# Kernel optimization log

Measured on AMD Instinct MI355X. Metric: run time of the kernel, lower is better.

Reference implementation:

```python
import jax, jax.numpy as jnp
import numpy as np

N = 100000       # nodes
E = 3200000      # edges
IN_DIM = 128
EDGE_DIM = 16
H = 64           # hidden_dim
L = 3            # num_layers
G = 256          # num graphs
BN_EPS = 1e-5


def setup_inputs() -> dict:
    key = jax.random.key(0)
    ks = jax.random.split(key, 16)
    x = jax.random.normal(ks[0], (N, IN_DIM), dtype=jnp.float32)
    edge_attr = jax.random.normal(ks[1], (E, EDGE_DIM), dtype=jnp.float32)
    edge_index = jax.random.randint(ks[2], (2, E), 0, N, dtype=jnp.int64)
    batch = jnp.sort(jax.random.randint(ks[3], (N,), 0, G, dtype=jnp.int64))
    s = 0.05
    np_w = jax.random.normal(ks[4], (IN_DIM, H), dtype=jnp.float32) * s
    np_b = jnp.zeros((H,), dtype=jnp.float32)
    ep_w = jax.random.normal(ks[5], (EDGE_DIM, H), dtype=jnp.float32) * s
    ep_b = jnp.zeros((H,), dtype=jnp.float32)
    mlp_w1 = jax.random.normal(ks[6], (L, H, H), dtype=jnp.float32) * s
    mlp_b1 = jnp.zeros((L, H), dtype=jnp.float32)
    mlp_w2 = jax.random.normal(ks[7], (L, H, H), dtype=jnp.float32) * s
    mlp_b2 = jnp.zeros((L, H), dtype=jnp.float32)
    bn_g = jnp.ones((L, H), dtype=jnp.float32)
    bn_b = jnp.zeros((L, H), dtype=jnp.float32)
    return {"x": x, "edge_attr": edge_attr, "edge_index": edge_index, "batch": batch,
            "np_w": np_w, "np_b": np_b, "ep_w": ep_w, "ep_b": ep_b,
            "mlp_w1": mlp_w1, "mlp_b1": mlp_b1, "mlp_w2": mlp_w2, "mlp_b2": mlp_b2,
            "bn_g": bn_g, "bn_b": bn_b}


def reference(x, edge_attr, edge_index, batch, np_w, np_b, ep_w, ep_b,
              mlp_w1, mlp_b1, mlp_w2, mlp_b2, bn_g, bn_b):
    h = x @ np_w + np_b                  # [N,H] node_proj
    e = edge_attr @ ep_w + ep_b          # [E,H] edge_proj
    src, dst = edge_index[0], edge_index[1]
    for l in range(L):
        # GINEConv (eps=0): MLP(x_i + sum_j ReLU(x_j + e_ij))
        msg = jax.nn.relu(h[src] + e)                          # [E,H] gather + edge add
        agg = jax.ops.segment_sum(msg, dst, num_segments=N)    # scatter-add
        z = h + agg
        z = jax.nn.relu(z @ mlp_w1[l] + mlp_b1[l]) @ mlp_w2[l] + mlp_b2[l]
        # BatchNorm1d over node dim (batch statistics, training-mode math)
        mu = jnp.mean(z, axis=0)
        var = jnp.mean((z - mu) ** 2, axis=0)
        z = (z - mu) * jax.lax.rsqrt(var + BN_EPS) * bn_g[l] + bn_b[l]
        h = jax.nn.relu(z)               # dropout omitted (deterministic reference)
    # global_mean_pool
    sums = jax.ops.segment_sum(h, batch, num_segments=G)
    cnts = jax.ops.segment_sum(jnp.ones((N,), dtype=h.dtype), batch, num_segments=G)
    graph_emb = sums / jnp.maximum(cnts, 1.0)[:, None]
    return h, graph_emb
```

## Files before the change

kernel.cpp:

```cpp
#include <hip/hip_runtime.h>
#include <hip/hip_bf16.h>

#define NN 100000
#define NE 3200000
#define IND 128
#define ED 16
#define HD 64
#define NL 3
#define NG 256
#define BN_EPS 1e-5f

#define NB 391
#define PBLK 512
#define PCHUNK 6250
#define MLP_BLOCKS 512

typedef unsigned int uint32;
typedef unsigned long long uint64;
typedef unsigned short ushort16;
typedef __attribute__((ext_vector_type(8))) short bf16x8;
typedef __attribute__((ext_vector_type(4))) float f32x4;

__device__ __forceinline__ ushort16 f2b(float f) {
    uint32 u = __float_as_uint(f);
    u = (u + 0x7fffu + ((u >> 16) & 1u)) >> 16;
    return (ushort16)u;
}
__device__ __forceinline__ float b2f(ushort16 b) {
    return __uint_as_float(((uint32)b) << 16);
}

__global__ __launch_bounds__(256) void k_node_proj(
    const float* __restrict__ x, const float* __restrict__ w,
    const float* __restrict__ b, ushort16* __restrict__ sb)
{
    __shared__ float xs[4][IND];
    const int wave = threadIdx.x >> 6, lane = threadIdx.x & 63;
    const int node = blockIdx.x * 4 + wave;
    const float2 v = *(const float2*)(x + (size_t)node * IND + lane * 2);
    ((float2*)xs[wave])[lane] = v;
    float acc = b[lane];
#pragma unroll
    for (int k = 0; k < IND; ++k)
        acc = fmaf(xs[wave][k], w[k * HD + lane], acc);
    sb[node * HD + lane] = f2b(acc);
}

__global__ __launch_bounds__(256) void k_p1(const int* __restrict__ ei,
                                            int* __restrict__ bh)
{
    __shared__ int hist[NB];
    const int t = threadIdx.x, blk = blockIdx.x;
    for (int i = t; i < NB; i += 256) hist[i] = 0;
    __syncthreads();
    const int base = blk * PCHUNK;
    for (int i = t; i < PCHUNK; i += 256)
        atomicAdd(&hist[ei[NE + base + i] >> 8], 1);
    __syncthreads();
    for (int i = t; i < NB; i += 256) bh[blk * NB + i] = hist[i];
}

__global__ __launch_bounds__(512) void k_p2(int* __restrict__ bh,
                                            int* __restrict__ bstart,
                                            int* __restrict__ rowptr)
{
    __shared__ int tot[NB];
    __shared__ int bsl[NB + 1];
    const int t = threadIdx.x;
    if (t < NB) {
        int s = 0;
        for (int blk = 0; blk < PBLK; ++blk) {
            const int idx = blk * NB + t;
            const int v = bh[idx];
            bh[idx] = s;
            s += v;
        }
        tot[t] = s;
    }
    __syncthreads();
    if (t == 0) {
        int run = 0;
        for (int b = 0; b < NB; ++b) { bsl[b] = run; run += tot[b]; }
        bsl[NB] = run;
    }
    __syncthreads();
    if (t < NB) {
        const int base = bsl[t];
        for (int blk = 0; blk < PBLK; ++blk) bh[blk * NB + t] += base;
        bstart[t] = base;
    }
    if (t == 0) { bstart[NB] = NE; rowptr[NN] = NE; }
}

__global__ __launch_bounds__(256) void k_p3(const int* __restrict__ ei,
                                            const int* __restrict__ bh,
                                            uint64* __restrict__ tmp)
{
    __shared__ int cursor[NB];
    const int t = threadIdx.x, blk = blockIdx.x;
    for (int i = t; i < NB; i += 256) cursor[i] = bh[blk * NB + i];
    __syncthreads();
    const int base = blk * PCHUNK;
    for (int i = t; i < PCHUNK; i += 256) {
        const int e = base + i;
        const int d = ei[NE + e];
        const int s = ei[e];
        const int pos = atomicAdd(&cursor[d >> 8], 1);
        tmp[pos] = (uint64)(uint32)d | ((uint64)(uint32)s << 17)
                 | ((uint64)(uint32)e << 34);
    }
}

__global__ __launch_bounds__(256) void k_p4(const uint64* __restrict__ tmp,
                                            const int* __restrict__ bstart,
                                            int* __restrict__ perm_src,
                                            int* __restrict__ perm_eid,
                                            int* __restrict__ rowptr)
{
    __shared__ int cnt[256], csave[256], cnt2[256];
    const int t = threadIdx.x, b = blockIdx.x;
    const int lo = bstart[b], hi = bstart[b + 1];
    cnt[t] = 0; cnt2[t] = 0;
    __syncthreads();
    for (int e = lo + t; e < hi; e += 256)
        atomicAdd(&cnt[(int)(tmp[e] & 0x1FFFF) & 255], 1);
    __syncthreads();
    csave[t] = cnt[t];
    __syncthreads();
    for (int off = 1; off < 256; off <<= 1) {
        const int v = (t >= off) ? cnt[t - off] : 0;
        __syncthreads();
        cnt[t] += v;
        __syncthreads();
    }
    const int excl = cnt[t] - csave[t];
    const int node = (b << 8) + t;
    if (node < NN) rowptr[node] = lo + excl;
    __syncthreads();
    csave[t] = excl;
    __syncthreads();
    for (int e = lo + t; e < hi; e += 256) {
        const uint64 u = tmp[e];
        const int loc = (int)(u & 0x1FFFF) & 255;
        const int r = atomicAdd(&cnt2[loc], 1);
        const int pos = lo + csave[loc] + r;
        perm_src[pos] = (int)((u >> 17) & 0x1FFFF);
        perm_eid[pos] = (int)(u >> 34);
    }
}

__global__ __launch_bounds__(256) void k_permute(
    const float* __restrict__ ea, const int* __restrict__ perm_eid,
    ushort16* __restrict__ ea_perm)
{
    const int pos = blockIdx.x * 256 + threadIdx.x;
    const int p = pos >> 2, q = pos & 3;
    const int eid = perm_eid[p];
    const float4 v = ((const float4*)(ea + (size_t)eid * ED))[q];
    ushort4 o;
    o.x = f2b(v.x); o.y = f2b(v.y); o.z = f2b(v.z); o.w = f2b(v.w);
    ((ushort4*)ea_perm)[pos] = o;
}

template <bool XFORM>
__global__ __launch_bounds__(256) void k_gather(
    const ushort16* __restrict__ eab, const int* __restrict__ perm_src,
    const int* __restrict__ rowptr,
    const float* __restrict__ epw, const float* __restrict__ epb,
    const ushort16* __restrict__ sb, const float* __restrict__ bnp,
    float* __restrict__ z)
{
    __shared__ float pe[4][64 * 17];
    const int lane = threadIdx.x & 63;
    const int wave = threadIdx.x >> 6;
    const int l15 = lane & 15, lg = lane >> 4;

    bf16x8 bfrag[4];
#pragma unroll
    for (int c = 0; c < 4; ++c) {
#pragma unroll
        for (int i = 0; i < 8; ++i) {
            const int k = lg * 8 + i;
            short v = 0;
            if (k < ED)       v = (short)f2b(epw[k * HD + c * 16 + l15]);
            else if (k == ED) v = (short)f2b(epb[c * 16 + l15]);
            bfrag[c][i] = v;
        }
    }
    const float tsc = XFORM ? bnp[lane] : 1.f;
    const float tsh = XFORM ? bnp[64 + lane] : 0.f;
    float* mype = pe[wave];

    const int node = __builtin_amdgcn_readfirstlane((blockIdx.x << 2) + wave);
    const int rs = rowptr[node];
    const int re = rowptr[node + 1];

    float acc = 0.f;
    for (int j = rs; j < re; j += 16) {
        int s[16];
#pragma unroll
        for (int m = 0; m < 16; ++m) {
            int idx = j + m;
            if (idx > NE - 1) idx = NE - 1;
            s[m] = perm_src[idx];
        }
        float hv[16];
#pragma unroll
        for (int m = 0; m < 16; ++m)
            hv[m] = b2f(sb[(size_t)s[m] * HD + lane]);

        bf16x8 a = {};
        if (lg < 2) {
            int row = j + l15;
            if (row > NE - 1) row = NE - 1;
            a = *(const bf16x8*)((const short*)eab + (size_t)row * ED + lg * 8);
        } else if (lg == 2) {
            a[0] = (short)0x3F80;
        }

        const f32x4 zero = {0.f, 0.f, 0.f, 0.f};
#pragma unroll
        for (int c = 0; c < 4; ++c) {
            const f32x4 d = __builtin_amdgcn_mfma_f32_16x16x32_bf16(
                a, bfrag[c], zero, 0, 0, 0);
            const int base = (c * 16 + l15) * 17 + lg * 4;
#pragma unroll
            for (int v = 0; v < 4; ++v) mype[base + v] = d[v];
        }

        if (XFORM) {
#pragma unroll
            for (int m = 0; m < 16; ++m)
                hv[m] = fmaxf(fmaf(hv[m], tsc, tsh), 0.f);
        }
        const int lim = re - j;
#pragma unroll
        for (int m = 0; m < 16; ++m) {
            if (m < lim)
                acc += fmaxf(hv[m] + mype[lane * 17 + m], 0.f);
        }
    }
    float u0 = b2f(sb[(size_t)node * HD + lane]);
    if (XFORM) u0 = fmaxf(fmaf(u0, tsc, tsh), 0.f);
    z[node * HD + lane] = acc + u0;
}

template <bool STORE_BF16>
__global__ __launch_bounds__(256) void k_mlp(
    float* __restrict__ z,
    const float* __restrict__ w1, const float* __restrict__ b1,
    const float* __restrict__ w2, const float* __restrict__ b2,
    ushort16* __restrict__ sb, float* __restrict__ part)
{
    __shared__ float z0s[4][HD];
    __shared__ float t1s[4][HD];
    __shared__ float red[4][2][HD];
    const int wave = threadIdx.x >> 6, lane = threadIdx.x & 63;
    const float vb1 = b1[lane], vb2 = b2[lane];
    float s1 = 0.f, s2 = 0.f;
    for (int node = blockIdx.x * 4 + wave; node < NN; node += MLP_BLOCKS * 4) {
        const int idx = node * HD + lane;
        z0s[wave][lane] = z[idx];
        float a = vb1;
#pragma unroll
        for (int k = 0; k < HD; ++k)
            a = fmaf(z0s[wave][k], w1[k * HD + lane], a);
        a = fmaxf(a, 0.f);
        t1s[wave][lane] = a;
        float o = vb2;
#pragma unroll
        for (int k = 0; k < HD; ++k)
            o = fmaf(t1s[wave][k], w2[k * HD + lane], o);
        if (STORE_BF16) sb[idx] = f2b(o);
        else            z[idx] = o;
        s1 += o;
        s2 += o * o;
    }
    red[wave][0][lane] = s1;
    red[wave][1][lane] = s2;
    __syncthreads();
    if (wave == 0) {
        float a = red[0][0][lane] + red[1][0][lane] + red[2][0][lane] + red[3][0][lane];
        float c = red[0][1][lane] + red[1][1][lane] + red[2][1][lane] + red[3][1][lane];
        part[blockIdx.x * 128 + lane] = a;
        part[blockIdx.x * 128 + 64 + lane] = c;
    }
}

__global__ __launch_bounds__(1024) void k_bn_final(
    const float* __restrict__ part,
    const float* __restrict__ g, const float* __restrict__ b,
    float* __restrict__ bnp)
{
    __shared__ float red[16][2][HD];
    const int c = threadIdx.x & 63;
    const int s = threadIdx.x >> 6;
    float s1 = 0.f, s2 = 0.f;
    for (int i = s; i < MLP_BLOCKS; i += 16) {
        s1 += part[i * 128 + c];
        s2 += part[i * 128 + 64 + c];
    }
    red[s][0][c] = s1;
    red[s][1][c] = s2;
    __syncthreads();
    if (s == 0) {
        float a = 0.f, q = 0.f;
#pragma unroll
        for (int i = 0; i < 16; ++i) { a += red[i][0][c]; q += red[i][1][c]; }
        const float mu  = a / (float)NN;
        const float var = q / (float)NN - mu * mu;
        const float rstd = rsqrtf(var + BN_EPS);
        const float sc = rstd * g[c];
        bnp[c] = sc;
        bnp[64 + c] = b[c] - mu * sc;
    }
}

__global__ __launch_bounds__(256) void k_pool_apply(
    const float* __restrict__ t2, const float* __restrict__ bnp,
    const int* __restrict__ batch,
    float* __restrict__ h, float* __restrict__ emb)
{
    __shared__ float red[4][HD];
    const int g = blockIdx.x;
    const int lane = threadIdx.x & 63;
    const int wave = threadIdx.x >> 6;
    int lo = 0, hi = NN;
    while (lo < hi) { int m = (lo + hi) >> 1; if (batch[m] < g) lo = m + 1; else hi = m; }
    const int start = lo;
    hi = NN;
    while (lo < hi) { int m = (lo + hi) >> 1; if (batch[m] <= g) lo = m + 1; else hi = m; }
    const int end = lo;
    const float sc = bnp[lane];
    const float sh = bnp[64 + lane];
    float acc = 0.f;
    for (int n = start + wave; n < end; n += 4) {
        const float v = fmaxf(fmaf(t2[(size_t)n * HD + lane], sc, sh), 0.f);
        h[(size_t)n * HD + lane] = v;
        acc += v;
    }
    red[wave][lane] = acc;
    __syncthreads();
    if (wave == 0) {
        const float a = red[0][lane] + red[1][lane] + red[2][lane] + red[3][lane];
        emb[g * HD + lane] = a / fmaxf((float)(end - start), 1.f);
    }
}

extern "C" void kernel_launch(void* const* d_in, const int* in_sizes, int n_in,
                              void* d_out, int out_size, void* d_ws, size_t ws_size,
                              hipStream_t stream)
{
    const float* x     = (const float*)d_in[0];
    const float* ea    = (const float*)d_in[1];
    const int*   ei    = (const int*)d_in[2];
    const int*   batch = (const int*)d_in[3];
    const float* np_w  = (const float*)d_in[4];
    const float* np_b  = (const float*)d_in[5];
    const float* ep_w  = (const float*)d_in[6];
    const float* ep_b  = (const float*)d_in[7];
    const float* w1    = (const float*)d_in[8];
    const float* b1    = (const float*)d_in[9];
    const float* w2    = (const float*)d_in[10];
    const float* b2    = (const float*)d_in[11];
    const float* bng   = (const float*)d_in[12];
    const float* bnb   = (const float*)d_in[13];

    float* h   = (float*)d_out;
    float* emb = h + (size_t)NN * HD;

    char* ws = (char*)d_ws;
    float*     agg      = (float*)    (ws);
    uint64*    tmp      = (uint64*)   (ws);
    float*     part     = (float*)    (ws + 25600000);
    float*     bnp      = (float*)    (ws + 26648576);
    int*       bh       = (int*)      (ws + 26650112);
    int*       bstart   = (int*)      (ws + 27450880);
    int*       rowptr   = (int*)      (ws + 27452448);
    ushort16*  sb       = (ushort16*) (ws + 27852464);
    int*       perm_src = (int*)      (ws + 40652464);
    int*       perm_eid = (int*)      (ws + 53452464);
    ushort16*  ea_perm  = (ushort16*) (ws + 66252464);

    k_node_proj<<<NN / 4, 256, 0, stream>>>(x, np_w, np_b, sb);

    k_p1<<<PBLK, 256, 0, stream>>>(ei, bh);
    k_p2<<<1, 512, 0, stream>>>(bh, bstart, rowptr);
    k_p3<<<PBLK, 256, 0, stream>>>(ei, bh, tmp);
    k_p4<<<NB, 256, 0, stream>>>(tmp, bstart, perm_src, perm_eid, rowptr);
    k_permute<<<NE * 4 / 256, 256, 0, stream>>>(ea, perm_eid, ea_perm);

    for (int l = 0; l < NL; ++l) {
        if (l == 0)
            k_gather<false><<<NN / 4, 256, 0, stream>>>(
                ea_perm, perm_src, rowptr, ep_w, ep_b, sb, bnp, agg);
        else
            k_gather<true><<<NN / 4, 256, 0, stream>>>(
                ea_perm, perm_src, rowptr, ep_w, ep_b, sb, bnp + (l - 1) * 128, agg);
        if (l < NL - 1)
            k_mlp<true><<<MLP_BLOCKS, 256, 0, stream>>>(
                agg, w1 + l * HD * HD, b1 + l * HD, w2 + l * HD * HD, b2 + l * HD,
                sb, part);
        else
            k_mlp<false><<<MLP_BLOCKS, 256, 0, stream>>>(
                agg, w1 + l * HD * HD, b1 + l * HD, w2 + l * HD * HD, b2 + l * HD,
                sb, part);
        k_bn_final<<<1, 1024, 0, stream>>>(part, bng + l * HD, bnb + l * HD, bnp + l * 128);
    }

    k_pool_apply<<<NG, 256, 0, stream>>>(agg, bnp + 2 * 128, batch, h, emb);
}
```

Measured before the change: 1.213 ms.

## Parallelize bucket prefix scan and fuse BN finalize into MLP via last-block ticket

Replaces the single-block serial column scan over 512x391 bucket histograms with a multi-block scan (one block per bucket) plus a small single-block scan of totals. Bucket base offsets are now added inside k_p3 instead of being folded into the histogram array. Also removes the separate k_bn_final launch per layer: the last MLP block to finish, found with an atomic ticket counter, reduces the partial sums and writes the BN scale and shift. This cuts a serial bottleneck and three launches, at the cost of an extra launch for the scan, threadfence and atomic overhead, and a counter that must be reset each run (done in node_proj).

```diff
diff --git a/kernel.cpp b/kernel.cpp
--- a/kernel.cpp
+++ b/kernel.cpp
@@ -32,8 +32,10 @@
 
 __global__ __launch_bounds__(256) void k_node_proj(
     const float* __restrict__ x, const float* __restrict__ w,
-    const float* __restrict__ b, ushort16* __restrict__ sb)
-{
+    const float* __restrict__ b, ushort16* __restrict__ sb,
+    int* __restrict__ cnt)
+{
+    if (blockIdx.x == 0 && threadIdx.x < NL) cnt[threadIdx.x] = 0;
     __shared__ float xs[4][IND];
     const int wave = threadIdx.x >> 6, lane = threadIdx.x & 63;
     const int node = blockIdx.x * 4 + wave;
@@ -60,45 +62,53 @@
     for (int i = t; i < NB; i += 256) bh[blk * NB + i] = hist[i];
 }
 
-__global__ __launch_bounds__(512) void k_p2(int* __restrict__ bh,
-                                            int* __restrict__ bstart,
-                                            int* __restrict__ rowptr)
-{
-    __shared__ int tot[NB];
-    __shared__ int bsl[NB + 1];
+__global__ __launch_bounds__(PBLK) void k_p2a(int* __restrict__ bh,
+                                              int* __restrict__ gtot)
+{
+    __shared__ int ps[PBLK];
+    const int b = blockIdx.x;
     const int t = threadIdx.x;
-    if (t < NB) {
-        int s = 0;
-        for (int blk = 0; blk < PBLK; ++blk) {
-            const int idx = blk * NB + t;
-            const int v = bh[idx];
-            bh[idx] = s;
-            s += v;
-        }
-        tot[t] = s;
-    }
-    __syncthreads();
-    if (t == 0) {
-        int run = 0;
-        for (int b = 0; b < NB; ++b) { bsl[b] = run; run += tot[b]; }
-        bsl[NB] = run;
-    }
-    __syncthreads();
-    if (t < NB) {
-        const int base = bsl[t];
-        for (int blk = 0; blk < PBLK; ++blk) bh[blk * NB + t] += base;
-        bstart[t] = base;
-    }
+    const int v = bh[t * NB + b];
+    ps[t] = v;
+    __syncthreads();
+    for (int off = 1; off < PBLK; off <<= 1) {
+        const int u = (t >= off) ? ps[t - off] : 0;
+        __syncthreads();
+        ps[t] += u;
+        __syncthreads();
+    }
+    bh[t * NB + b] = ps[t] - v;
+    if (t == PBLK - 1) gtot[b] = ps[t];
+}
+
+__global__ __launch_bounds__(512) void k_p2b(const int* __restrict__ gtot,
+                                             int* __restrict__ bstart,
+                                             int* __restrict__ rowptr)
+{
+    __shared__ int ps[512];
+    const int t = threadIdx.x;
+    const int v = (t < NB) ? gtot[t] : 0;
+    ps[t] = v;
+    __syncthreads();
+    for (int off = 1; off < 512; off <<= 1) {
+        const int u = (t >= off) ? ps[t - off] : 0;
+        __syncthreads();
+        ps[t] += u;
+        __syncthreads();
+    }
+    if (t < NB) bstart[t] = ps[t] - v;
     if (t == 0) { bstart[NB] = NE; rowptr[NN] = NE; }
 }
 
 __global__ __launch_bounds__(256) void k_p3(const int* __restrict__ ei,
                                             const int* __restrict__ bh,
+                                            const int* __restrict__ bstart,
                                             uint64* __restrict__ tmp)
 {
     __shared__ int cursor[NB];
     const int t = threadIdx.x, blk = blockIdx.x;
-    for (int i = t; i < NB; i += 256) cursor[i] = bh[blk * NB + i];
+    for (int i = t; i < NB; i += 256)
+        cursor[i] = bh[blk * NB + i] + bstart[i];
     __syncthreads();
     const int base = blk * PCHUNK;
     for (int i = t; i < PCHUNK; i += 256) {
@@ -250,7 +260,9 @@
     float* __restrict__ z,
     const float* __restrict__ w1, const float* __restrict__ b1,
     const float* __restrict__ w2, const float* __restrict__ b2,
-    ushort16* __restrict__ sb, float* __restrict__ part)
+    const float* __restrict__ bng, const float* __restrict__ bnb,
+    ushort16* __restrict__ sb, float* __restrict__ part,
+    int* __restrict__ cnt, float* __restrict__ bnp)
 {
     __shared__ float z0s[4][HD];
     __shared__ float t1s[4][HD];
@@ -285,34 +297,31 @@
         part[blockIdx.x * 128 + lane] = a;
         part[blockIdx.x * 128 + 64 + lane] = c;
     }
-}
-
-__global__ __launch_bounds__(1024) void k_bn_final(
-    const float* __restrict__ part,
-    const float* __restrict__ g, const float* __restrict__ b,
-    float* __restrict__ bnp)
-{
-    __shared__ float red[16][2][HD];
-    const int c = threadIdx.x & 63;
-    const int s = threadIdx.x >> 6;
-    float s1 = 0.f, s2 = 0.f;
-    for (int i = s; i < MLP_BLOCKS; i += 16) {
-        s1 += part[i * 128 + c];
-        s2 += part[i * 128 + 64 + c];
-    }
-    red[s][0][c] = s1;
-    red[s][1][c] = s2;
-    __syncthreads();
-    if (s == 0) {
-        float a = 0.f, q = 0.f;
-#pragma unroll
-        for (int i = 0; i < 16; ++i) { a += red[i][0][c]; q += red[i][1][c]; }
-        const float mu  = a / (float)NN;
-        const float var = q / (float)NN - mu * mu;
-        const float rstd = rsqrtf(var + BN_EPS);
-        const float sc = rstd * g[c];
-        bnp[c] = sc;
-        bnp[64 + c] = b[c] - mu * sc;
+    __shared__ int ticket;
+    __threadfence();
+    if (threadIdx.x == 0) ticket = atomicAdd(cnt, 1);
+    __syncthreads();
+    if (ticket == MLP_BLOCKS - 1) {
+        __threadfence();
+        __shared__ float r2[2][128];
+        const int c = threadIdx.x & 127;
+        const int g = threadIdx.x >> 7;
+        float s = 0.f;
+        for (int r = g; r < MLP_BLOCKS; r += 2)
+            s += part[r * 128 + c];
+        r2[g][c] = s;
+        __syncthreads();
+        if (threadIdx.x < 64) {
+            const int cc = threadIdx.x;
+            const float T1 = r2[0][cc] + r2[1][cc];
+            const float T2 = r2[0][cc + 64] + r2[1][cc + 64];
+            const float mu  = T1 / (float)NN;
+            const float var = T2 / (float)NN - mu * mu;
+            const float rstd = rsqrtf(var + BN_EPS);
+            const float sc = rstd * bng[cc];
+            bnp[cc] = sc;
+            bnp[64 + cc] = bnb[cc] - mu * sc;
+        }
     }
 }
 
@@ -373,6 +382,8 @@
     float*     agg      = (float*)    (ws);
     uint64*    tmp      = (uint64*)   (ws);
     float*     part     = (float*)    (ws + 25600000);
+    int*       gtot     = (int*)      (ws + 25600000);
+    int*       cnt      = (int*)      (ws + 26100000);
     float*     bnp      = (float*)    (ws + 26648576);
     int*       bh       = (int*)      (ws + 26650112);
     int*       bstart   = (int*)      (ws + 27450880);
@@ -382,11 +393,12 @@
     int*       perm_eid = (int*)      (ws + 53452464);
     ushort16*  ea_perm  = (ushort16*) (ws + 66252464);
 
-    k_node_proj<<<NN / 4, 256, 0, stream>>>(x, np_w, np_b, sb);
+    k_node_proj<<<NN / 4, 256, 0, stream>>>(x, np_w, np_b, sb, cnt);
 
     k_p1<<<PBLK, 256, 0, stream>>>(ei, bh);
-    k_p2<<<1, 512, 0, stream>>>(bh, bstart, rowptr);
-    k_p3<<<PBLK, 256, 0, stream>>>(ei, bh, tmp);
+    k_p2a<<<NB, PBLK, 0, stream>>>(bh, gtot);
+    k_p2b<<<1, 512, 0, stream>>>(gtot, bstart, rowptr);
+    k_p3<<<PBLK, 256, 0, stream>>>(ei, bh, bstart, tmp);
     k_p4<<<NB, 256, 0, stream>>>(tmp, bstart, perm_src, perm_eid, rowptr);
     k_permute<<<NE * 4 / 256, 256, 0, stream>>>(ea, perm_eid, ea_perm);
 
@@ -400,12 +412,11 @@
         if (l < NL - 1)
             k_mlp<true><<<MLP_BLOCKS, 256, 0, stream>>>(
                 agg, w1 + l * HD * HD, b1 + l * HD, w2 + l * HD * HD, b2 + l * HD,
-                sb, part);
+                bng + l * HD, bnb + l * HD, sb, part, cnt + l, bnp + l * 128);
         else
             k_mlp<false><<<MLP_BLOCKS, 256, 0, stream>>>(
                 agg, w1 + l * HD * HD, b1 + l * HD, w2 + l * HD * HD, b2 + l * HD,
-                sb, part);
-        k_bn_final<<<1, 1024, 0, stream>>>(part, bng + l * HD, bnb + l * HD, bnp + l * 128);
+                bng + l * HD, bnb + l * HD, sb, part, cnt + l, bnp + l * 128);
     }
 
     k_pool_apply<<<NG, 256, 0, stream>>>(agg, bnp + 2 * 128, batch, h, emb);
```

Result: slower. 1.419 ms (+16.9%).
